# Optimization experiments

Hardware: AMD Instinct MI355X
Metric: run time of the kernel (lower is better)

## Reference

```python
import jax, jax.numpy as jnp
import numpy as np

DIM = 2048
NUM_HEADS = 16
HEAD_DIM = DIM // NUM_HEADS  # 128
B, L = 2, 2048


def setup_inputs() -> dict:
    key = jax.random.key(0)
    ks = jax.random.split(key, 5)
    x = jax.random.normal(ks[0], (B, L, DIM), dtype=jnp.float32)
    # genuine RoPE tables: inv_freq over half the head dim
    half = HEAD_DIM // 2
    inv_freq = 1.0 / (10000.0 ** (jnp.arange(half, dtype=jnp.float32) / half))
    ang = jnp.arange(L, dtype=jnp.float32)[:, None] * inv_freq[None, :]  # (L, half)
    cos = jnp.cos(ang)[:, None, :]  # (L, 1, half) broadcasts over (B,L,H,half)
    sin = jnp.sin(ang)[:, None, :]
    def dw_init(k, shape):
        fan_in, fan_out = shape
        std = 1.0 / np.sqrt(fan_in) * min(1.0, np.sqrt(fan_out / fan_in))
        return jax.random.normal(k, shape, dtype=jnp.float32) * std
    Wq = dw_init(ks[1], (DIM, DIM))
    Wk = dw_init(ks[2], (DIM, HEAD_DIM))
    Wv = dw_init(ks[3], (DIM, HEAD_DIM))
    Wo = dw_init(ks[4], (DIM, DIM))  # random instead of zeros so output is nontrivial
    return {"x": x, "cos": cos, "sin": sin, "Wq": Wq, "Wk": Wk, "Wv": Wv, "Wo": Wo}


def apply_rotary_emb(x, cos, sin):
    x1, x2 = jnp.split(x, 2, axis=-1)
    return jnp.concatenate([x1 * cos + x2 * sin, x1 * -sin + x2 * cos], axis=-1)


def rms_norm(x):
    return x * jax.lax.rsqrt(jnp.mean(x * x, axis=-1, keepdims=True) + 1e-6)


def reference(x, cos, sin, Wq, Wk, Wv, Wo):
    Bb, Ll, _ = x.shape
    q = (x @ Wq).reshape(Bb, Ll, NUM_HEADS, HEAD_DIM)  # (B,L,H,D)
    k = (x @ Wk)  # (B,L,D)  single KV head (MQA)
    v = (x @ Wv)  # (B,L,D)
    q = rms_norm(apply_rotary_emb(q, cos, sin))
    k = rms_norm(apply_rotary_emb(k[:, :, None, :], cos, sin))[:, :, 0, :]  # (B,L,D)
    scale = 1.0 / jnp.sqrt(jnp.asarray(HEAD_DIM, dtype=x.dtype))
    # scores without materializing broadcasted K: (B,H,Lq,Lk)
    scores = jnp.einsum('bqhd,bkd->bhqk', q, k) * scale
    causal = jnp.tril(jnp.ones((Ll, Ll), dtype=jnp.bool_))
    scores = jnp.where(causal[None, None], scores, jnp.asarray(-jnp.inf, dtype=scores.dtype))
    attn = jax.nn.softmax(scores, axis=-1)
    out = jnp.einsum('bhqk,bkd->bqhd', attn, v).reshape(Bb, Ll, DIM)
    return out @ Wo
```

## Files before the change

kernel.cpp:

```cpp
#include <hip/hip_runtime.h>

#define DIM 2048
#define NH 16
#define HD 128
#define BB 2
#define LL 2048
#define MROWS (BB * LL)
#define NKV 2304
#define NT 32

typedef __attribute__((ext_vector_type(8))) short short8;
typedef __attribute__((ext_vector_type(4))) float floatx4;

__device__ inline ushort f2bf(float f) {
    union { float f; unsigned u; } v; v.f = f;
    unsigned r = v.u + 0x7FFFu + ((v.u >> 16) & 1u);
    return (ushort)(r >> 16);
}

__device__ __forceinline__ ushort f2bf_fast(float f) {
    __bf16 h = (__bf16)f;
    return __builtin_bit_cast(unsigned short, h);
}

#define GL16(g, l)                                                         \
    __builtin_amdgcn_global_load_lds(                                      \
        (const __attribute__((address_space(1))) unsigned int*)(g),        \
        (__attribute__((address_space(3))) unsigned int*)(l), 16, 0, 0)

__device__ __forceinline__ short8 ld8(const ushort* p) {
    return *reinterpret_cast<const short8*>(p);
}

__global__ __launch_bounds__(256) void conv_bf16(const float* __restrict__ in,
                                                 ushort* __restrict__ out) {
    size_t i = ((size_t)blockIdx.x * 256 + threadIdx.x) * 8;
    float4 a = *reinterpret_cast<const float4*>(in + i);
    float4 b = *reinterpret_cast<const float4*>(in + i + 4);
    ushort o[8] = {f2bf(a.x), f2bf(a.y), f2bf(a.z), f2bf(a.w),
                   f2bf(b.x), f2bf(b.y), f2bf(b.z), f2bf(b.w)};
    *reinterpret_cast<uint4*>(out + i) = *reinterpret_cast<uint4*>(o);
}

__global__ __launch_bounds__(256) void wprep(const float* __restrict__ Wq,
                                             const float* __restrict__ Wk,
                                             const float* __restrict__ Wv,
                                             const float* __restrict__ Wo,
                                             ushort* __restrict__ Wcatt,
                                             ushort* __restrict__ Wot) {
    __shared__ ushort T[64][72];
    const int bid = blockIdx.x;
    const float* in;
    ushort* out;
    int in_ld, c0, r0;
    const int out_ld = 2048;
    if (bid < 1024) {
        in = Wq; out = Wcatt; in_ld = 2048;
        c0 = (bid & 31) * 64; r0 = (bid >> 5) * 64;
    } else if (bid < 2048) {
        int t = bid - 1024;
        in = Wo; out = Wot; in_ld = 2048;
        c0 = (t & 31) * 64; r0 = (t >> 5) * 64;
    } else if (bid < 2112) {
        int t = bid - 2048;
        in = Wk; out = Wcatt + (size_t)2048 * 2048; in_ld = 128;
        c0 = (t & 1) * 64; r0 = (t >> 1) * 64;
    } else {
        int t = bid - 2112;
        in = Wv; out = Wcatt + (size_t)2176 * 2048; in_ld = 128;
        c0 = (t & 1) * 64; r0 = (t >> 1) * 64;
    }
    const int tid = threadIdx.x;
#pragma unroll
    for (int rep = 0; rep < 4; ++rep) {
        int idx = tid + rep * 256;
        int r = idx >> 4, c4 = idx & 15;
        float4 f = *reinterpret_cast<const float4*>(
            in + (size_t)(r0 + r) * in_ld + c0 + c4 * 4);
        T[r][c4 * 4 + 0] = f2bf(f.x);
        T[r][c4 * 4 + 1] = f2bf(f.y);
        T[r][c4 * 4 + 2] = f2bf(f.z);
        T[r][c4 * 4 + 3] = f2bf(f.w);
    }
    __syncthreads();
#pragma unroll
    for (int rep = 0; rep < 4; ++rep) {
        int idx = tid + rep * 256;
        int cr = idx >> 4, rc4 = idx & 15;
        uint a0 = (uint)T[rc4 * 4 + 0][cr] | ((uint)T[rc4 * 4 + 1][cr] << 16);
        uint a1 = (uint)T[rc4 * 4 + 2][cr] | ((uint)T[rc4 * 4 + 3][cr] << 16);
        uint2 val = {a0, a1};
        *reinterpret_cast<uint2*>(
            out + (size_t)(c0 + cr) * out_ld + r0 + rc4 * 4) = val;
    }
}

template <int U>
__device__ __forceinline__ void stage_unit(const ushort* __restrict__ A,
                                           const ushort* __restrict__ Bt,
                                           ushort* lbase, uint offA, uint offB,
                                           int t) {
    if (t >= NT) return;
    const ushort* g = (U < 2) ? Bt : A;
    uint off = ((U < 2) ? offB : offA) + ((U & 1) ? 128u * 2048u : 0u) +
               (uint)t * 64u;
    ushort* l = lbase + U * 8192;
    GL16(g + off, l + (size_t)threadIdx.x * 8);
    GL16(g + off + 64u * 2048u, l + (size_t)(threadIdx.x + 512) * 8);
}

__global__ __launch_bounds__(512)
__attribute__((amdgpu_waves_per_eu(2, 2)))
void gemm8p(const ushort* __restrict__ A,
            const ushort* __restrict__ Bt,
            float* __restrict__ Y, int N) {
    __shared__ __attribute__((aligned(16))) ushort lds[65536];
    const int tid = threadIdx.x;
    const int lane = tid & 63;
    const int w = tid >> 6;
    const int wm = w >> 2, wn = w & 3;
    const int col = lane & 15, quad = lane >> 4;
    const int sel = col & 7;
    const int m0 = blockIdx.y * 256, n0 = blockIdx.x * 256;

    const int r0 = tid >> 3;
    const int gc0 = (tid & 7) ^ (r0 & 7);
    const uint offA = (uint)(m0 + r0) * 2048u + (uint)gc0 * 8u;
    const uint offB = (uint)(n0 + r0) * 2048u + (uint)gc0 * 8u;

    floatx4 acc[8][4];
#pragma unroll
    for (int mt = 0; mt < 8; ++mt)
#pragma unroll
        for (int nt = 0; nt < 4; ++nt) acc[mt][nt] = (floatx4){0.f, 0.f, 0.f, 0.f};

    const int aoff0 = (2 + wm) * 8192 + col * 64;
    const int boff0 = (wn >> 1) * 8192 + ((wn & 1) * 64 + col) * 64;
    const int koff0 = (quad ^ sel) * 8;
    const int koff1 = ((4 + quad) ^ sel) * 8;

    stage_unit<0>(A, Bt, lds, offA, offB, 0);
    stage_unit<1>(A, Bt, lds, offA, offB, 0);
    stage_unit<2>(A, Bt, lds, offA, offB, 0);
    stage_unit<3>(A, Bt, lds, offA, offB, 0);
    stage_unit<0>(A, Bt, lds + 32768, offA, offB, 1);
    stage_unit<1>(A, Bt, lds + 32768, offA, offB, 1);
    asm volatile("s_waitcnt vmcnt(4)" ::: "memory");
    __builtin_amdgcn_s_barrier();

#pragma unroll 2
    for (int t = 0; t < NT; ++t) {
        ushort* lb = lds + (t & 1) * 32768;
        ushort* lbn = lds + ((t + 1) & 1) * 32768;

        short8 a0[4], b0[4];
#pragma unroll
        for (int mt = 0; mt < 4; ++mt)
            a0[mt] = ld8(lb + aoff0 + mt * 1024 + koff0);
#pragma unroll
        for (int nt = 0; nt < 4; ++nt)
            b0[nt] = ld8(lb + boff0 + nt * 1024 + koff0);
        stage_unit<2>(A, Bt, lbn, offA, offB, t + 1);
        stage_unit<3>(A, Bt, lbn, offA, offB, t + 1);
        __builtin_amdgcn_s_barrier();
        asm volatile("s_waitcnt lgkmcnt(0)" ::: "memory");
        __builtin_amdgcn_s_setprio(1);
#pragma unroll
        for (int mt = 0; mt < 4; ++mt)
#pragma unroll
            for (int nt = 0; nt < 4; ++nt)
                acc[mt][nt] = __builtin_amdgcn_mfma_f32_16x16x32_bf16(
                    a0[mt], b0[nt], acc[mt][nt], 0, 0, 0);
        __builtin_amdgcn_s_setprio(0);
        __builtin_amdgcn_s_barrier();

        short8 a1[4];
#pragma unroll
        for (int mt = 0; mt < 4; ++mt)
            a1[mt] = ld8(lb + aoff0 + (4 + mt) * 1024 + koff0);
        __builtin_amdgcn_s_barrier();
        asm volatile("s_waitcnt lgkmcnt(0)" ::: "memory");
        __builtin_amdgcn_s_setprio(1);
#pragma unroll
        for (int mt = 0; mt < 4; ++mt)
#pragma unroll
            for (int nt = 0; nt < 4; ++nt)
                acc[4 + mt][nt] = __builtin_amdgcn_mfma_f32_16x16x32_bf16(
                    a1[mt], b0[nt], acc[4 + mt][nt], 0, 0, 0);
        __builtin_amdgcn_s_setprio(0);
        __builtin_amdgcn_s_barrier();

        short8 a2[4], b1[4];
#pragma unroll
        for (int mt = 0; mt < 4; ++mt)
            a2[mt] = ld8(lb + aoff0 + mt * 1024 + koff1);
#pragma unroll
        for (int nt = 0; nt < 4; ++nt)
            b1[nt] = ld8(lb + boff0 + nt * 1024 + koff1);
        __builtin_amdgcn_s_barrier();
        asm volatile("s_waitcnt lgkmcnt(0)" ::: "memory");
        __builtin_amdgcn_s_setprio(1);
#pragma unroll
        for (int mt = 0; mt < 4; ++mt)
#pragma unroll
            for (int nt = 0; nt < 4; ++nt)
                acc[mt][nt] = __builtin_amdgcn_mfma_f32_16x16x32_bf16(
                    a2[mt], b1[nt], acc[mt][nt], 0, 0, 0);
        __builtin_amdgcn_s_setprio(0);
        __builtin_amdgcn_s_barrier();

        short8 a3[4];
#pragma unroll
        for (int mt = 0; mt < 4; ++mt)
            a3[mt] = ld8(lb + aoff0 + (4 + mt) * 1024 + koff1);
        stage_unit<0>(A, Bt, lb, offA, offB, t + 2);
        stage_unit<1>(A, Bt, lb, offA, offB, t + 2);
        __builtin_amdgcn_s_barrier();
        if (t < NT - 2)
            asm volatile("s_waitcnt vmcnt(4) lgkmcnt(0)" ::: "memory");
        else
            asm volatile("s_waitcnt vmcnt(0) lgkmcnt(0)" ::: "memory");
        __builtin_amdgcn_s_setprio(1);
#pragma unroll
        for (int mt = 0; mt < 4; ++mt)
#pragma unroll
            for (int nt = 0; nt < 4; ++nt)
                acc[4 + mt][nt] = __builtin_amdgcn_mfma_f32_16x16x32_bf16(
                    a3[mt], b1[nt], acc[4 + mt][nt], 0, 0, 0);
        __builtin_amdgcn_s_setprio(0);
        __builtin_amdgcn_s_barrier();
    }

#pragma unroll
    for (int mt = 0; mt < 8; ++mt)
#pragma unroll
        for (int nt = 0; nt < 4; ++nt)
#pragma unroll
            for (int rr = 0; rr < 4; ++rr)
                Y[(size_t)(m0 + wm * 128 + mt * 16 + quad * 4 + rr) * N + n0 +
                  wn * 64 + nt * 16 + col] = acc[mt][nt][rr];
}

__global__ __launch_bounds__(256) void rope_rms_bf16(const float* __restrict__ in,
                                                     ushort* __restrict__ outb,
                                                     const float* __restrict__ cosb,
                                                     const float* __restrict__ sinb,
                                                     int heads, int nrows,
                                                     int in_ld) {
    int row = blockIdx.x * 4 + (threadIdx.x >> 6);
    int lane = threadIdx.x & 63;
    if (row >= nrows) return;
    int token = row / heads, head = row % heads;
    int l = token & (LL - 1);
    const float* p = in + (size_t)token * in_ld + head * HD;
    float x1 = p[lane];
    float x2 = p[lane + 64];
    float c = cosb[l * 64 + lane];
    float s = sinb[l * 64 + lane];
    float o1 = x1 * c + x2 * s;
    float o2 = -x1 * s + x2 * c;
    float ss = o1 * o1 + o2 * o2;
#pragma unroll
    for (int off = 32; off > 0; off >>= 1) ss += __shfl_xor(ss, off);
    float r = rsqrtf(ss * (1.0f / 128.0f) + 1e-6f);
    outb[(size_t)row * HD + lane] = f2bf(o1 * r);
    outb[(size_t)row * HD + lane + 64] = f2bf(o2 * r);
}

__global__ __launch_bounds__(256) void vtrans(const float* __restrict__ v,
                                              ushort* __restrict__ vt,
                                              int in_ld) {
    __shared__ ushort T[64][72];
    const int l0 = blockIdx.x * 64, d0 = blockIdx.y * 64, b = blockIdx.z;
    const int tid = threadIdx.x;
#pragma unroll
    for (int rep = 0; rep < 4; ++rep) {
        int idx = tid + rep * 256;
        int r = idx >> 4, c4 = idx & 15;
        float4 f = *reinterpret_cast<const float4*>(
            v + (size_t)(b * LL + l0 + r) * in_ld + d0 + c4 * 4);
        T[r][c4 * 4 + 0] = f2bf(f.x);
        T[r][c4 * 4 + 1] = f2bf(f.y);
        T[r][c4 * 4 + 2] = f2bf(f.z);
        T[r][c4 * 4 + 3] = f2bf(f.w);
    }
    __syncthreads();
#pragma unroll
    for (int rep = 0; rep < 4; ++rep) {
        int idx = tid + rep * 256;
        int dr = idx >> 4, lc4 = idx & 15;
        uint a0 = (uint)T[lc4 * 4 + 0][dr] | ((uint)T[lc4 * 4 + 1][dr] << 16);
        uint a1 = (uint)T[lc4 * 4 + 2][dr] | ((uint)T[lc4 * 4 + 3][dr] << 16);
        uint2 val = {a0, a1};
        *reinterpret_cast<uint2*>(
            vt + (size_t)(b * HD + d0 + dr) * LL + l0 + lc4 * 4) = val;
    }
}

__global__ __launch_bounds__(256) void flash_mfma(const ushort* __restrict__ qb,
                                                  const ushort* __restrict__ kb,
                                                  const ushort* __restrict__ vt,
                                                  ushort* __restrict__ aob) {
    __shared__ ushort Ks[64 * 128];
    __shared__ ushort VTs[128 * 64];
    __shared__ ushort Ps[4][16][68];

    const int tid = threadIdx.x;
    const int w = tid >> 6, lane = tid & 63;
    const int col = lane & 15, quad = lane >> 4;
    const int pairIdx = blockIdx.x, bh = blockIdx.y;
    const int b = bh >> 4, h = bh & 15;
    const int sel = col & 7;
    const float scl2 = 0.08838834764831845f * 1.44269504088896340736f;
    const float M2 = 11.5f * 1.44269504088896340736f;

    const int ksr[4] = {(tid + 0) >> 4, (tid + 256) >> 4, (tid + 512) >> 4,
                        (tid + 768) >> 4};
    const int vsr[4] = {(tid + 0) >> 3, (tid + 256) >> 3, (tid + 512) >> 3,
                        (tid + 768) >> 3};

    for (int sp = 0; sp < 2; ++sp) {
        const int qt = sp ? (31 - pairIdx) : pairIdx;
        const int q0 = qt * 64;

        const ushort* qrow =
            qb + ((size_t)(b * LL + q0 + w * 16 + col) * NH + h) * HD;
        short8 aq[4];
#pragma unroll
        for (int kc = 0; kc < 4; ++kc)
            aq[kc] = *reinterpret_cast<const short8*>(qrow + kc * 32 + quad * 8);

        float lrow[4] = {0.f, 0.f, 0.f, 0.f};
        floatx4 oacc[8];
#pragma unroll
        for (int dt = 0; dt < 8; ++dt) oacc[dt] = (floatx4){0.f, 0.f, 0.f, 0.f};

        const int ntiles = qt + 1;
        for (int kt = 0; kt < ntiles; ++kt) {
            const int k0 = kt * 64;
            __syncthreads();
#pragma unroll
            for (int rep = 0; rep < 4; ++rep) {
                int slot = tid + rep * 256;
                int r = ksr[rep];
                int gc = (slot & 15) ^ (r & 7);
                GL16(kb + (size_t)(b * LL + k0 + r) * HD + gc * 8,
                     Ks + (size_t)slot * 8);
            }
#pragma unroll
            for (int rep = 0; rep < 4; ++rep) {
                int slot = tid + rep * 256;
                int r = vsr[rep];
                int gc = (slot & 7) ^ (r & 7);
                GL16(vt + (size_t)(b * HD + r) * LL + k0 + gc * 8,
                     VTs + (size_t)slot * 8);
            }
            __syncthreads();

            floatx4 sacc[4];
#pragma unroll
            for (int nt = 0; nt < 4; ++nt)
                sacc[nt] = (floatx4){0.f, 0.f, 0.f, 0.f};
            __builtin_amdgcn_s_setprio(1);
#pragma unroll
            for (int nt = 0; nt < 4; ++nt) {
#pragma unroll
                for (int kc = 0; kc < 4; ++kc) {
                    short8 bk = *reinterpret_cast<const short8*>(
                        &Ks[(nt * 16 + col) * 128 +
                            ((kc * 4 + quad) ^ sel) * 8]);
                    sacc[nt] = __builtin_amdgcn_mfma_f32_16x16x32_bf16(
                        aq[kc], bk, sacc[nt], 0, 0, 0);
                }
            }
            __builtin_amdgcn_s_setprio(0);

            float psum[4] = {0.f, 0.f, 0.f, 0.f};
            if (kt == qt) {
#pragma unroll
                for (int nt = 0; nt < 4; ++nt) {
                    int kj = k0 + nt * 16 + col;
#pragma unroll
                    for (int rr = 0; rr < 4; ++rr) {
                        int qi = q0 + w * 16 + quad * 4 + rr;
                        float p = exp2f(fmaf(sacc[nt][rr], scl2, -M2));
                        p = (kj <= qi) ? p : 0.0f;
                        sacc[nt][rr] = p;
                        psum[rr] += p;
                    }
                }
            } else {
#pragma unroll
                for (int nt = 0; nt < 4; ++nt)
#pragma unroll
                    for (int rr = 0; rr < 4; ++rr) {
                        float p = exp2f(fmaf(sacc[nt][rr], scl2, -M2));
                        sacc[nt][rr] = p;
                        psum[rr] += p;
                    }
            }
#pragma unroll
            for (int rr = 0; rr < 4; ++rr) lrow[rr] += psum[rr];

#pragma unroll
            for (int nt = 0; nt < 4; ++nt)
#pragma unroll
                for (int rr = 0; rr < 4; ++rr)
                    Ps[w][quad * 4 + rr][nt * 16 + col] =
                        f2bf_fast(sacc[nt][rr]);
            asm volatile("s_waitcnt lgkmcnt(0)" ::: "memory");

#pragma unroll
            for (int kt2 = 0; kt2 < 2; ++kt2) {
                short8 ap = *reinterpret_cast<const short8*>(
                    &Ps[w][col][kt2 * 32 + quad * 8]);
                __builtin_amdgcn_s_setprio(1);
#pragma unroll
                for (int dt = 0; dt < 8; ++dt) {
                    short8 bv = *reinterpret_cast<const short8*>(
                        &VTs[(dt * 16 + col) * 64 +
                             ((kt2 * 4 + quad) ^ sel) * 8]);
                    oacc[dt] = __builtin_amdgcn_mfma_f32_16x16x32_bf16(
                        ap, bv, oacc[dt], 0, 0, 0);
                }
                __builtin_amdgcn_s_setprio(0);
            }
        }

#pragma unroll
        for (int off = 1; off < 16; off <<= 1)
#pragma unroll
            for (int rr = 0; rr < 4; ++rr)
                lrow[rr] += __shfl_xor(lrow[rr], off);
        float inv[4];
#pragma unroll
        for (int rr = 0; rr < 4; ++rr) inv[rr] = 1.0f / lrow[rr];
#pragma unroll
        for (int dt = 0; dt < 8; ++dt)
#pragma unroll
            for (int rr = 0; rr < 4; ++rr)
                aob[((size_t)(b * LL + q0 + w * 16 + quad * 4 + rr) * NH + h) *
                        HD + dt * 16 + col] =
                    f2bf_fast(oacc[dt][rr] * inv[rr]);
    }
}

extern "C" void kernel_launch(void* const* d_in, const int* in_sizes, int n_in,
                              void* d_out, int out_size, void* d_ws,
                              size_t ws_size, hipStream_t stream) {
    const float* x    = (const float*)d_in[0];
    const float* cosb = (const float*)d_in[1];
    const float* sinb = (const float*)d_in[2];
    const float* Wq   = (const float*)d_in[3];
    const float* Wk   = (const float*)d_in[4];
    const float* Wv   = (const float*)d_in[5];
    const float* Wo   = (const float*)d_in[6];
    float* out = (float*)d_out;

    float* qkv  = (float*)d_ws;
    ushort* xb  = (ushort*)(qkv + (size_t)MROWS * NKV);
    ushort* qb  = xb + (size_t)MROWS * DIM;
    ushort* kb  = qb + (size_t)MROWS * DIM;
    ushort* vt  = kb + (size_t)MROWS * HD;
    ushort* aob = vt + (size_t)MROWS * HD;
    ushort* Wcatt = aob + (size_t)MROWS * DIM;
    ushort* Wot   = Wcatt + (size_t)NKV * DIM;

    conv_bf16<<<dim3(MROWS * DIM / (256 * 8)), 256, 0, stream>>>(x, xb);
    wprep<<<dim3(2176), 256, 0, stream>>>(Wq, Wk, Wv, Wo, Wcatt, Wot);

    gemm8p<<<dim3(NKV / 256, MROWS / 256), 512, 0, stream>>>(xb, Wcatt, qkv,
                                                             NKV);

    rope_rms_bf16<<<dim3(MROWS * NH / 4), 256, 0, stream>>>(
        qkv, qb, cosb, sinb, NH, MROWS * NH, NKV);
    rope_rms_bf16<<<dim3(MROWS / 4), 256, 0, stream>>>(
        qkv + DIM, kb, cosb, sinb, 1, MROWS, NKV);
    vtrans<<<dim3(LL / 64, 2, BB), 256, 0, stream>>>(qkv + DIM + HD, vt, NKV);

    flash_mfma<<<dim3(LL / 128, BB * NH), 256, 0, stream>>>(qb, kb, vt, aob);

    gemm8p<<<dim3(DIM / 256, MROWS / 256), 512, 0, stream>>>(aob, Wot, out,
                                                             DIM);
}
```

Measured before the change: 317.3 us.

## Simplify GEMM main loop from 8-phase to 2-phase schedule with one barrier

Replaces the 8-phase ping-pong GEMM loop, which had many barriers and split the global prefetch across two iterations, with a 2-phase loop. Each iteration loads all A and B fragments for half of the K tile, issues the full next-tile prefetch, runs 32 MFMAs, repeats for the second half, then waits for all loads and hits a single barrier. This removes per-phase barriers and waits, but gives up the finer interleaving of LDS reads, global loads and MFMAs. It also raises register pressure from holding 8 A fragments at once.

```diff
diff --git a/kernel.cpp b/kernel.cpp
--- a/kernel.cpp
+++ b/kernel.cpp
@@ -111,7 +111,7 @@
 
 __global__ __launch_bounds__(512)
 __attribute__((amdgpu_waves_per_eu(2, 2)))
-void gemm8p(const ushort* __restrict__ A,
+void gemm2p(const ushort* __restrict__ A,
             const ushort* __restrict__ Bt,
             float* __restrict__ Y, int N) {
     __shared__ __attribute__((aligned(16))) ushort lds[65536];
@@ -143,9 +143,7 @@
     stage_unit<1>(A, Bt, lds, offA, offB, 0);
     stage_unit<2>(A, Bt, lds, offA, offB, 0);
     stage_unit<3>(A, Bt, lds, offA, offB, 0);
-    stage_unit<0>(A, Bt, lds + 32768, offA, offB, 1);
-    stage_unit<1>(A, Bt, lds + 32768, offA, offB, 1);
-    asm volatile("s_waitcnt vmcnt(4)" ::: "memory");
+    asm volatile("s_waitcnt vmcnt(0)" ::: "memory");
     __builtin_amdgcn_s_barrier();
 
 #pragma unroll 2
@@ -153,81 +151,42 @@
         ushort* lb = lds + (t & 1) * 32768;
         ushort* lbn = lds + ((t + 1) & 1) * 32768;
 
-        short8 a0[4], b0[4];
-#pragma unroll
-        for (int mt = 0; mt < 4; ++mt)
+        short8 a0[8], b0[4];
+#pragma unroll
+        for (int mt = 0; mt < 8; ++mt)
             a0[mt] = ld8(lb + aoff0 + mt * 1024 + koff0);
 #pragma unroll
         for (int nt = 0; nt < 4; ++nt)
             b0[nt] = ld8(lb + boff0 + nt * 1024 + koff0);
+        stage_unit<0>(A, Bt, lbn, offA, offB, t + 1);
+        stage_unit<1>(A, Bt, lbn, offA, offB, t + 1);
         stage_unit<2>(A, Bt, lbn, offA, offB, t + 1);
         stage_unit<3>(A, Bt, lbn, offA, offB, t + 1);
-        __builtin_amdgcn_s_barrier();
-        asm volatile("s_waitcnt lgkmcnt(0)" ::: "memory");
         __builtin_amdgcn_s_setprio(1);
 #pragma unroll
-        for (int mt = 0; mt < 4; ++mt)
+        for (int mt = 0; mt < 8; ++mt)
 #pragma unroll
             for (int nt = 0; nt < 4; ++nt)
                 acc[mt][nt] = __builtin_amdgcn_mfma_f32_16x16x32_bf16(
                     a0[mt], b0[nt], acc[mt][nt], 0, 0, 0);
         __builtin_amdgcn_s_setprio(0);
-        __builtin_amdgcn_s_barrier();
-
-        short8 a1[4];
-#pragma unroll
-        for (int mt = 0; mt < 4; ++mt)
-            a1[mt] = ld8(lb + aoff0 + (4 + mt) * 1024 + koff0);
-        __builtin_amdgcn_s_barrier();
-        asm volatile("s_waitcnt lgkmcnt(0)" ::: "memory");
-        __builtin_amdgcn_s_setprio(1);
-#pragma unroll
-        for (int mt = 0; mt < 4; ++mt)
-#pragma unroll
-            for (int nt = 0; nt < 4; ++nt)
-                acc[4 + mt][nt] = __builtin_amdgcn_mfma_f32_16x16x32_bf16(
-                    a1[mt], b0[nt], acc[4 + mt][nt], 0, 0, 0);
-        __builtin_amdgcn_s_setprio(0);
-        __builtin_amdgcn_s_barrier();
-
-        short8 a2[4], b1[4];
-#pragma unroll
-        for (int mt = 0; mt < 4; ++mt)
-            a2[mt] = ld8(lb + aoff0 + mt * 1024 + koff1);
+
+        short8 a1[8], b1[4];
+#pragma unroll
+        for (int mt = 0; mt < 8; ++mt)
+            a1[mt] = ld8(lb + aoff0 + mt * 1024 + koff1);
 #pragma unroll
         for (int nt = 0; nt < 4; ++nt)
             b1[nt] = ld8(lb + boff0 + nt * 1024 + koff1);
-        __builtin_amdgcn_s_barrier();
-        asm volatile("s_waitcnt lgkmcnt(0)" ::: "memory");
         __builtin_amdgcn_s_setprio(1);
 #pragma unroll
-        for (int mt = 0; mt < 4; ++mt)
+        for (int mt = 0; mt < 8; ++mt)
 #pragma unroll
             for (int nt = 0; nt < 4; ++nt)
                 acc[mt][nt] = __builtin_amdgcn_mfma_f32_16x16x32_bf16(
-                    a2[mt], b1[nt], acc[mt][nt], 0, 0, 0);
+                    a1[mt], b1[nt], acc[mt][nt], 0, 0, 0);
         __builtin_amdgcn_s_setprio(0);
-        __builtin_amdgcn_s_barrier();
-
-        short8 a3[4];
-#pragma unroll
-        for (int mt = 0; mt < 4; ++mt)
-            a3[mt] = ld8(lb + aoff0 + (4 + mt) * 1024 + koff1);
-        stage_unit<0>(A, Bt, lb, offA, offB, t + 2);
-        stage_unit<1>(A, Bt, lb, offA, offB, t + 2);
-        __builtin_amdgcn_s_barrier();
-        if (t < NT - 2)
-            asm volatile("s_waitcnt vmcnt(4) lgkmcnt(0)" ::: "memory");
-        else
-            asm volatile("s_waitcnt vmcnt(0) lgkmcnt(0)" ::: "memory");
-        __builtin_amdgcn_s_setprio(1);
-#pragma unroll
-        for (int mt = 0; mt < 4; ++mt)
-#pragma unroll
-            for (int nt = 0; nt < 4; ++nt)
-                acc[4 + mt][nt] = __builtin_amdgcn_mfma_f32_16x16x32_bf16(
-                    a3[mt], b1[nt], acc[4 + mt][nt], 0, 0, 0);
-        __builtin_amdgcn_s_setprio(0);
+        asm volatile("s_waitcnt vmcnt(0)" ::: "memory");
         __builtin_amdgcn_s_barrier();
     }
 
@@ -469,7 +428,7 @@
     conv_bf16<<<dim3(MROWS * DIM / (256 * 8)), 256, 0, stream>>>(x, xb);
     wprep<<<dim3(2176), 256, 0, stream>>>(Wq, Wk, Wv, Wo, Wcatt, Wot);
 
-    gemm8p<<<dim3(NKV / 256, MROWS / 256), 512, 0, stream>>>(xb, Wcatt, qkv,
+    gemm2p<<<dim3(NKV / 256, MROWS / 256), 512, 0, stream>>>(xb, Wcatt, qkv,
                                                              NKV);
 
     rope_rms_bf16<<<dim3(MROWS * NH / 4), 256, 0, stream>>>(
@@ -480,6 +439,6 @@
 
     flash_mfma<<<dim3(LL / 128, BB * NH), 256, 0, stream>>>(qb, kb, vt, aob);
 
-    gemm8p<<<dim3(DIM / 256, MROWS / 256), 512, 0, stream>>>(aob, Wot, out,
+    gemm2p<<<dim3(DIM / 256, MROWS / 256), 512, 0, stream>>>(aob, Wot, out,
                                                              DIM);
 }
```

New measurement: 306.3 us. 3.5% less time.
